# Kernel tuning notes

Measured on AMD Instinct MI355X. Metric: run time of the kernel, lower is better.

## Reference

```python
import jax, jax.numpy as jnp
import numpy as np

B, D_MODEL, L = 4, 512, 1024
N_HEADS = 8

def setup_inputs() -> dict:
    key = jax.random.key(0)
    ks = jax.random.split(key, 7)
    s = 1.0 / np.sqrt(D_MODEL)
    return {
        "queries": jax.random.normal(ks[0], (B, D_MODEL, 3, L), dtype=jnp.float32),
        "keys":    jax.random.normal(ks[1], (B, D_MODEL, 3, L), dtype=jnp.float32),
        "values":  jax.random.normal(ks[2], (B, D_MODEL, 3, L), dtype=jnp.float32),
        "Wq": jax.random.normal(ks[3], (D_MODEL, D_MODEL), dtype=jnp.float32) * s,
        "Wk": jax.random.normal(ks[4], (D_MODEL, D_MODEL), dtype=jnp.float32) * s,
        "Wv": jax.random.normal(ks[5], (D_MODEL, D_MODEL), dtype=jnp.float32) * s,
        "Wo": jax.random.normal(ks[6], (D_MODEL, D_MODEL), dtype=jnp.float32) * s,
        "n_heads": N_HEADS,
    }

def reference(queries, keys, values, Wq, Wk, Wv, Wo, n_heads):
    # inputs: [B, D, 3, L]; VNLinear = bias-free linear over channel dim D
    Bv, D, _, Lv = queries.shape
    H = n_heads
    dh = D // H
    # project and reshape to [B, L, H, dh, 3]
    def proj(x, W):
        y = jnp.einsum('ed,bdvl->blev', W, x)          # [B, L, D, 3]
        return y.reshape(Bv, Lv, H, dh, 3)
    q = proj(queries, Wq)
    k = proj(keys, Wk)
    v = proj(values, Wv)
    # score over extra vector axis v: [B, H, 3, L, S]
    score = jnp.einsum('blhdv,bshdv->bhvls', q, k)
    scale = 1.0 / jnp.sqrt(jnp.asarray(3.0, score.dtype))  # original grabs last dim (=3)
    attn = jax.nn.softmax(scale * score, axis=-1)
    # weighted values: [B, L, 3, H, dh] -> [B, L, 3, D]
    V = jnp.einsum('bhvls,bshdv->blvhd', attn, v).reshape(Bv, Lv, 3, D)
    # output projection on channel dim: result [B, D, 3, L]
    out = jnp.einsum('ed,blvd->bevl', Wo, V)
    return out, attn
```

## Files before the change

### kernel.cpp

```cpp
#include <hip/hip_runtime.h>
#include <hip/hip_bf16.h>

typedef __hip_bfloat16 bf16;
using bf16x8 = __attribute__((ext_vector_type(8))) short;
using f32x4  = __attribute__((ext_vector_type(4))) float;

#define Bn 4
#define Dm 512
#define Hh 8
#define V3 3
#define Lq 1024
#define NM (Bn*Hh*V3)

#define WPITCH 144

__device__ __forceinline__ unsigned short f2bf(float x) {
    bf16 h = __float2bfloat16(x);
    return *reinterpret_cast<unsigned short*>(&h);
}
__device__ __forceinline__ float bfbits2f(unsigned short u) {
    return __uint_as_float((unsigned)u << 16);
}

constexpr float SCALE = 0.57735026919f;

__global__ __launch_bounds__(256, 4) void proj_all_kernel(
    const float* __restrict__ xq, const float* __restrict__ xk,
    const float* __restrict__ xv,
    const float* __restrict__ Wq, const float* __restrict__ Wk,
    const float* __restrict__ Wv,
    unsigned short* __restrict__ Qh, unsigned short* __restrict__ Ql,
    unsigned short* __restrict__ Kh, unsigned short* __restrict__ Kl,
    unsigned short* __restrict__ Vt)
{
    __shared__ unsigned char Wlds[2 * 64 * WPITCH];
    unsigned char* LWh = Wlds;
    unsigned char* LWl = Wlds + 64 * WPITCH;

    const int fid = (blockIdx.z * gridDim.y + blockIdx.y) * gridDim.x + blockIdx.x;
    const int nid = (fid & 7) * 576 + (fid >> 3);
    const int x_  = nid & 15;
    const int y_  = (nid >> 4) & 7;
    const int zz  = nid >> 7;
    const int pid = zz / 12;
    const int pl  = zz % 12;
    const int b   = pl / V3;
    const int v   = pl % V3;

    const float* xsrc = (pid == 0) ? xq : (pid == 1) ? xk : xv;
    const float* W    = (pid == 0) ? Wq : (pid == 1) ? Wk : Wv;

    const int l0 = x_ * 64;
    const int e0 = y_ * 64;
    const int m  = (b * Hh + y_) * V3 + v;

    const int tid  = threadIdx.x;
    const int w    = tid >> 6;
    const int ln   = tid & 63;
    const int ln15 = ln & 15;
    const int lq   = ln >> 4;
    const int wl   = w * 16 + ln15;

    const float* xbase = xsrc + (size_t)b * Dm * V3 * Lq + (size_t)v * Lq + l0 + wl;

    f32x4 acc[4];
    #pragma unroll
    for (int i = 0; i < 4; ++i) acc[i] = (f32x4)0.f;

    for (int ph = 0; ph < 8; ++ph) {
        const int d0 = ph * 64;

        float xraw[16];
        #pragma unroll
        for (int kq = 0; kq < 2; ++kq)
            #pragma unroll
            for (int j = 0; j < 8; ++j)
                xraw[kq * 8 + j] =
                    xbase[(size_t)(d0 + kq * 32 + lq * 8 + j) * (V3 * Lq)];

        __syncthreads();
        #pragma unroll
        for (int q2 = 0; q2 < 4; ++q2) {
            int idx  = tid + q2 * 256;
            int row  = idx >> 4;
            int dloc = (idx & 15) * 4;
            float4 wv4 = *reinterpret_cast<const float4*>(
                W + (size_t)(e0 + row) * Dm + d0 + dloc);
            float wz[4] = {wv4.x, wv4.y, wv4.z, wv4.w};
            union { unsigned short u[4]; uint2 v2; } hp, lp;
            #pragma unroll
            for (int e = 0; e < 4; ++e) {
                hp.u[e] = f2bf(wz[e]);
                lp.u[e] = f2bf(wz[e] - bfbits2f(hp.u[e]));
            }
            *reinterpret_cast<uint2*>(LWh + row * WPITCH + dloc * 2) = hp.v2;
            *reinterpret_cast<uint2*>(LWl + row * WPITCH + dloc * 2) = lp.v2;
        }
        __syncthreads();

        bf16x8 xh[2], xl[2];
        #pragma unroll
        for (int kq = 0; kq < 2; ++kq)
            #pragma unroll
            for (int j = 0; j < 8; ++j) {
                float xv_ = xraw[kq * 8 + j];
                unsigned short hs = f2bf(xv_);
                unsigned short ls = f2bf(xv_ - bfbits2f(hs));
                xh[kq][j] = (short)hs;
                xl[kq][j] = (short)ls;
            }

        #pragma unroll
        for (int lt = 0; lt < 4; ++lt) {
            int erow = lt * 16 + ln15;
            #pragma unroll
            for (int kq = 0; kq < 2; ++kq) {
                bf16x8 wh = *reinterpret_cast<const bf16x8*>(
                    LWh + erow * WPITCH + kq * 64 + lq * 16);
                bf16x8 wl_ = *reinterpret_cast<const bf16x8*>(
                    LWl + erow * WPITCH + kq * 64 + lq * 16);
                acc[lt] = __builtin_amdgcn_mfma_f32_16x16x32_bf16(wh,  xh[kq], acc[lt], 0, 0, 0);
                acc[lt] = __builtin_amdgcn_mfma_f32_16x16x32_bf16(wl_, xh[kq], acc[lt], 0, 0, 0);
                acc[lt] = __builtin_amdgcn_mfma_f32_16x16x32_bf16(wh,  xl[kq], acc[lt], 0, 0, 0);
            }
        }
    }

    if (pid < 2) {
        unsigned short* Oh_ = (pid == 0) ? Qh : Kh;
        unsigned short* Ol_ = (pid == 0) ? Ql : Kl;
        size_t rowbase = ((size_t)m * Lq + l0 + wl) * 64;
        #pragma unroll
        for (int lt = 0; lt < 4; ++lt) {
            union { unsigned short u[4]; uint2 v2; } hp, lp;
            #pragma unroll
            for (int r = 0; r < 4; ++r) {
                float y = acc[lt][r];
                hp.u[r] = f2bf(y);
                lp.u[r] = f2bf(y - bfbits2f(hp.u[r]));
            }
            *reinterpret_cast<uint2*>(Oh_ + rowbase + lt * 16 + lq * 4) = hp.v2;
            *reinterpret_cast<uint2*>(Ol_ + rowbase + lt * 16 + lq * 4) = lp.v2;
        }
    } else {
        #pragma unroll
        for (int lt = 0; lt < 4; ++lt)
            #pragma unroll
            for (int r = 0; r < 4; ++r) {
                int dd = lt * 16 + lq * 4 + r;
                Vt[(((size_t)(m * 64 + dd)) << 10) + l0 + wl] = f2bf(acc[lt][r]);
            }
    }
}

__device__ __forceinline__ void stage_tile64(
    unsigned char* dst, const unsigned short* __restrict__ src,
    size_t row_stride, int tid)
{
    #pragma unroll
    for (int q = 0; q < 2; ++q) {
        int u = tid + q * 256;
        int row = u >> 3, off = u & 7;
        uint4 d = *reinterpret_cast<const uint4*>(src + (size_t)row * row_stride + off * 8);
        *reinterpret_cast<uint4*>(dst + ((row * 128 + off * 16) ^ ((row & 7) << 4))) = d;
    }
}

__global__ __launch_bounds__(256) void fused_attn_kernel(
    const unsigned short* __restrict__ Qh, const unsigned short* __restrict__ Ql,
    const unsigned short* __restrict__ Kh, const unsigned short* __restrict__ Kl,
    const unsigned short* __restrict__ Vt, float* __restrict__ attn_out,
    unsigned short* __restrict__ Ot)
{
    __shared__ float4 ldsf4[2128];
    unsigned char* L   = (unsigned char*)ldsf4;
    unsigned char* Lkh = L;
    unsigned char* Lkl = L + 8192;
    unsigned char* Lvt = L + 16384;
    unsigned char* Lp  = L + 24576;
    float* rowsumW = (float*)(L + 32768);
    float* invrow  = (float*)(L + 33792);

    const int fid = blockIdx.y * gridDim.x + blockIdx.x;
    const int nid = (fid & 7) * 192 + (fid >> 3);
    const int m  = nid >> 4;
    const int l0 = (nid & 15) * 64;

    const int tid = threadIdx.x;
    const int w    = tid >> 6;
    const int ln   = tid & 63;
    const int ln15 = ln & 15;
    const int lq   = ln >> 4;
    const int sc   = w * 16;

    stage_tile64(Lkh, Qh + ((size_t)m * Lq + l0) * 64, 64, tid);
    stage_tile64(Lkl, Ql + ((size_t)m * Lq + l0) * 64, 64, tid);
    __syncthreads();
    bf16x8 qfh[4][2], qfl[4][2];
    #pragma unroll
    for (int lt = 0; lt < 4; ++lt) {
        int row = lt * 16 + ln15;
        #pragma unroll
        for (int kq = 0; kq < 2; ++kq) {
            int byte = (row * 128 + kq * 64 + lq * 16) ^ ((row & 7) << 4);
            qfh[lt][kq] = *reinterpret_cast<const bf16x8*>(Lkh + byte);
            qfl[lt][kq] = *reinterpret_cast<const bf16x8*>(Lkl + byte);
        }
    }
    __syncthreads();

    const size_t mbase = (size_t)m * Lq * Lq;
    const unsigned short* Khm = Kh + (size_t)m * Lq * 64;
    const unsigned short* Klm = Kl + (size_t)m * Lq * 64;
    const unsigned short* Vtm = Vt + (((size_t)m * 64) << 10);

    float lsum[4][4] = {};
    for (int s0 = 0; s0 < Lq; s0 += 64) {
        stage_tile64(Lkh, Khm + (size_t)s0 * 64, 64, tid);
        stage_tile64(Lkl, Klm + (size_t)s0 * 64, 64, tid);
        __syncthreads();
        bf16x8 bh[2], bl[2];
        #pragma unroll
        for (int kq = 0; kq < 2; ++kq) {
            int row = sc + ln15;
            int byte = (row * 128 + kq * 64 + lq * 16) ^ ((row & 7) << 4);
            bh[kq] = *reinterpret_cast<const bf16x8*>(Lkh + byte);
            bl[kq] = *reinterpret_cast<const bf16x8*>(Lkl + byte);
        }
        #pragma unroll
        for (int lt = 0; lt < 4; ++lt) {
            f32x4 c = (f32x4)0.f;
            #pragma unroll
            for (int kq = 0; kq < 2; ++kq) {
                c = __builtin_amdgcn_mfma_f32_16x16x32_bf16(qfh[lt][kq], bh[kq], c, 0, 0, 0);
                c = __builtin_amdgcn_mfma_f32_16x16x32_bf16(qfl[lt][kq], bh[kq], c, 0, 0, 0);
                c = __builtin_amdgcn_mfma_f32_16x16x32_bf16(qfh[lt][kq], bl[kq], c, 0, 0, 0);
            }
            #pragma unroll
            for (int r = 0; r < 4; ++r)
                lsum[lt][r] += __expf(c[r] * SCALE);
        }
        __syncthreads();
    }
    #pragma unroll
    for (int lt = 0; lt < 4; ++lt)
        #pragma unroll
        for (int r = 0; r < 4; ++r) {
            float vv = lsum[lt][r];
            vv += __shfl_xor(vv, 1);
            vv += __shfl_xor(vv, 2);
            vv += __shfl_xor(vv, 4);
            vv += __shfl_xor(vv, 8);
            if (ln15 == 0) rowsumW[w * 64 + lt * 16 + lq * 4 + r] = vv;
        }
    __syncthreads();
    if (tid < 64)
        invrow[tid] = 1.0f / (rowsumW[tid] + rowsumW[64 + tid] +
                              rowsumW[128 + tid] + rowsumW[192 + tid]);
    __syncthreads();

    f32x4 o[4];
    o[0] = (f32x4)0.f; o[1] = (f32x4)0.f; o[2] = (f32x4)0.f; o[3] = (f32x4)0.f;

    for (int s0 = 0; s0 < Lq; s0 += 64) {
        stage_tile64(Lkh, Khm + (size_t)s0 * 64, 64, tid);
        stage_tile64(Lkl, Klm + (size_t)s0 * 64, 64, tid);
        stage_tile64(Lvt, Vtm + s0, 1024, tid);
        __syncthreads();
        bf16x8 bh[2], bl[2];
        #pragma unroll
        for (int kq = 0; kq < 2; ++kq) {
            int row = sc + ln15;
            int byte = (row * 128 + kq * 64 + lq * 16) ^ ((row & 7) << 4);
            bh[kq] = *reinterpret_cast<const bf16x8*>(Lkh + byte);
            bl[kq] = *reinterpret_cast<const bf16x8*>(Lkl + byte);
        }
        #pragma unroll
        for (int lt = 0; lt < 4; ++lt) {
            f32x4 c = (f32x4)0.f;
            #pragma unroll
            for (int kq = 0; kq < 2; ++kq) {
                c = __builtin_amdgcn_mfma_f32_16x16x32_bf16(qfh[lt][kq], bh[kq], c, 0, 0, 0);
                c = __builtin_amdgcn_mfma_f32_16x16x32_bf16(qfl[lt][kq], bh[kq], c, 0, 0, 0);
                c = __builtin_amdgcn_mfma_f32_16x16x32_bf16(qfh[lt][kq], bl[kq], c, 0, 0, 0);
            }
            #pragma unroll
            for (int r = 0; r < 4; ++r) {
                int l = lt * 16 + lq * 4 + r;
                float p = __expf(c[r] * SCALE) * invrow[l];
                attn_out[mbase + (size_t)(l0 + l) * Lq + s0 + sc + ln15] = p;
                int byte = (l * 128 + (sc + ln15) * 2) ^ ((l & 7) << 4);
                *reinterpret_cast<unsigned short*>(Lp + byte) = f2bf(p);
            }
        }
        __syncthreads();
        {
            int prow = w * 16 + ln15;
            #pragma unroll
            for (int kq = 0; kq < 2; ++kq) {
                bf16x8 pa = *reinterpret_cast<const bf16x8*>(
                    Lp + ((prow * 128 + kq * 64 + lq * 16) ^ ((prow & 7) << 4)));
                #pragma unroll
                for (int nt = 0; nt < 4; ++nt) {
                    int vrow = nt * 16 + ln15;
                    bf16x8 vb = *reinterpret_cast<const bf16x8*>(
                        Lvt + ((vrow * 128 + kq * 64 + lq * 16) ^ ((vrow & 7) << 4)));
                    o[nt] = __builtin_amdgcn_mfma_f32_16x16x32_bf16(pa, vb, o[nt], 0, 0, 0);
                }
            }
        }
        __syncthreads();
    }

    #pragma unroll
    for (int nt = 0; nt < 4; ++nt) {
        int dd = nt * 16 + ln15;
        #pragma unroll
        for (int r = 0; r < 4; ++r) {
            int l = w * 16 + lq * 4 + r;
            Ot[((size_t)m * Lq + l0 + l) * 64 + dd] = f2bf(o[nt][r]);
        }
    }
}

__global__ __launch_bounds__(256, 4) void oproj_kernel(
    const float* __restrict__ Wo, const unsigned short* __restrict__ Ot,
    float* __restrict__ out)
{
    __shared__ unsigned char Wlds[2 * 64 * WPITCH];
    unsigned char* LWh = Wlds;
    unsigned char* LWl = Wlds + 64 * WPITCH;

    const int fid = (blockIdx.z * gridDim.y + blockIdx.y) * gridDim.x + blockIdx.x;
    const int nid = (fid & 7) * 192 + (fid >> 3);
    const int x_  = nid & 15;
    const int y_  = (nid >> 4) & 7;
    const int pl  = nid >> 7;
    const int b   = pl / V3;
    const int v   = pl % V3;

    const int l0 = x_ * 64;
    const int e0 = y_ * 64;

    const int tid  = threadIdx.x;
    const int w    = tid >> 6;
    const int ln   = tid & 63;
    const int ln15 = ln & 15;
    const int lq   = ln >> 4;
    const int wl   = w * 16 + ln15;

    f32x4 acc[4];
    #pragma unroll
    for (int i = 0; i < 4; ++i) acc[i] = (f32x4)0.f;

    for (int h = 0; h < Hh; ++h) {
        const int m = (b * Hh + h) * V3 + v;

        size_t obase = ((size_t)m * Lq + l0 + wl) * 64;
        bf16x8 ob0 = *reinterpret_cast<const bf16x8*>(Ot + obase + lq * 8);
        bf16x8 ob1 = *reinterpret_cast<const bf16x8*>(Ot + obase + 32 + lq * 8);

        __syncthreads();
        #pragma unroll
        for (int q2 = 0; q2 < 4; ++q2) {
            int idx  = tid + q2 * 256;
            int row  = idx >> 4;
            int dloc = (idx & 15) * 4;
            float4 wv4 = *reinterpret_cast<const float4*>(
                Wo + (size_t)(e0 + row) * Dm + h * 64 + dloc);
            float wz[4] = {wv4.x, wv4.y, wv4.z, wv4.w};
            union { unsigned short u[4]; uint2 v2; } hp, lp;
            #pragma unroll
            for (int e = 0; e < 4; ++e) {
                hp.u[e] = f2bf(wz[e]);
                lp.u[e] = f2bf(wz[e] - bfbits2f(hp.u[e]));
            }
            *reinterpret_cast<uint2*>(LWh + row * WPITCH + dloc * 2) = hp.v2;
            *reinterpret_cast<uint2*>(LWl + row * WPITCH + dloc * 2) = lp.v2;
        }
        __syncthreads();

        #pragma unroll
        for (int lt = 0; lt < 4; ++lt) {
            int erow = lt * 16 + ln15;
            #pragma unroll
            for (int kq = 0; kq < 2; ++kq) {
                bf16x8 wh = *reinterpret_cast<const bf16x8*>(
                    LWh + erow * WPITCH + kq * 64 + lq * 16);
                bf16x8 wl_ = *reinterpret_cast<const bf16x8*>(
                    LWl + erow * WPITCH + kq * 64 + lq * 16);
                bf16x8 ob = kq ? ob1 : ob0;
                acc[lt] = __builtin_amdgcn_mfma_f32_16x16x32_bf16(wh,  ob, acc[lt], 0, 0, 0);
                acc[lt] = __builtin_amdgcn_mfma_f32_16x16x32_bf16(wl_, ob, acc[lt], 0, 0, 0);
            }
        }
    }

    #pragma unroll
    for (int lt = 0; lt < 4; ++lt)
        #pragma unroll
        for (int r = 0; r < 4; ++r) {
            int e = e0 + lt * 16 + lq * 4 + r;
            out[((size_t)(b * Dm + e) * V3 + v) * Lq + l0 + wl] = acc[lt][r];
        }
}

extern "C" void kernel_launch(void* const* d_in, const int* in_sizes, int n_in,
                              void* d_out, int out_size, void* d_ws, size_t ws_size,
                              hipStream_t stream)
{
    const float* q  = (const float*)d_in[0];
    const float* k  = (const float*)d_in[1];
    const float* vv = (const float*)d_in[2];
    const float* Wq = (const float*)d_in[3];
    const float* Wk = (const float*)d_in[4];
    const float* Wv = (const float*)d_in[5];
    const float* Wo = (const float*)d_in[6];

    float* out      = (float*)d_out;
    float* attn_out = out + (size_t)Bn * Dm * V3 * Lq;

    char* w = (char*)d_ws;
    unsigned short* Qh = (unsigned short*)(w);
    unsigned short* Ql = (unsigned short*)(w + 12582912);
    unsigned short* Kh = (unsigned short*)(w + 25165824);
    unsigned short* Kl = (unsigned short*)(w + 37748736);
    unsigned short* Vt = (unsigned short*)(w + 50331648);
    unsigned short* Ot = (unsigned short*)(w + 62914560);

    dim3 b256(256);

    proj_all_kernel<<<dim3(16, 8, 36), b256, 0, stream>>>(
        q, k, vv, Wq, Wk, Wv, Qh, Ql, Kh, Kl, Vt);

    fused_attn_kernel<<<dim3(16, NM), b256, 0, stream>>>(
        Qh, Ql, Kh, Kl, Vt, attn_out, Ot);

    oproj_kernel<<<dim3(16, 8, 12), b256, 0, stream>>>(Wo, Ot, out);
}
```

Measured before the change: 696.3 us.

## Prefetch K/V tiles into registers and coalesce attention-matrix stores via LDS

Splits tile staging into a global-to-register load and a register-to-LDS write, so the next K/Kl/Vt tile is fetched while the current one is being computed. It also removes one barrier and raises wave priority around the MFMA blocks. The attention probabilities are now written to global memory as wide float4 stores read back from the bf16 P tile in LDS, instead of scattered 4-byte stores. The trade-off is that the stored attn output is rounded to bf16 rather than kept in full fp32, which reduces accuracy.

```diff
diff --git a/kernel.cpp b/kernel.cpp
--- a/kernel.cpp
+++ b/kernel.cpp
@@ -153,16 +153,24 @@
     }
 }
 
-__device__ __forceinline__ void stage_tile64(
-    unsigned char* dst, const unsigned short* __restrict__ src,
-    size_t row_stride, int tid)
+__device__ __forceinline__ void tile_load(
+    uint4* r, const unsigned short* __restrict__ src, size_t row_stride, int tid)
 {
     #pragma unroll
     for (int q = 0; q < 2; ++q) {
         int u = tid + q * 256;
         int row = u >> 3, off = u & 7;
-        uint4 d = *reinterpret_cast<const uint4*>(src + (size_t)row * row_stride + off * 8);
-        *reinterpret_cast<uint4*>(dst + ((row * 128 + off * 16) ^ ((row & 7) << 4))) = d;
+        r[q] = *reinterpret_cast<const uint4*>(src + (size_t)row * row_stride + off * 8);
+    }
+}
+__device__ __forceinline__ void tile_write(
+    const uint4* r, unsigned char* dst, int tid)
+{
+    #pragma unroll
+    for (int q = 0; q < 2; ++q) {
+        int u = tid + q * 256;
+        int row = u >> 3, off = u & 7;
+        *reinterpret_cast<uint4*>(dst + ((row * 128 + off * 16) ^ ((row & 7) << 4))) = r[q];
     }
 }
 
@@ -193,8 +201,13 @@
     const int lq   = ln >> 4;
     const int sc   = w * 16;
 
-    stage_tile64(Lkh, Qh + ((size_t)m * Lq + l0) * 64, 64, tid);
-    stage_tile64(Lkl, Ql + ((size_t)m * Lq + l0) * 64, 64, tid);
+    {
+        uint4 rq[2];
+        tile_load(rq, Qh + ((size_t)m * Lq + l0) * 64, 64, tid);
+        tile_write(rq, Lkh, tid);
+        tile_load(rq, Ql + ((size_t)m * Lq + l0) * 64, 64, tid);
+        tile_write(rq, Lkl, tid);
+    }
     __syncthreads();
     bf16x8 qfh[4][2], qfl[4][2];
     #pragma unroll
@@ -207,7 +220,6 @@
             qfl[lt][kq] = *reinterpret_cast<const bf16x8*>(Lkl + byte);
         }
     }
-    __syncthreads();
 
     const size_t mbase = (size_t)m * Lq * Lq;
     const unsigned short* Khm = Kh + (size_t)m * Lq * 64;
@@ -215,32 +227,46 @@
     const unsigned short* Vtm = Vt + (((size_t)m * 64) << 10);
 
     float lsum[4][4] = {};
-    for (int s0 = 0; s0 < Lq; s0 += 64) {
-        stage_tile64(Lkh, Khm + (size_t)s0 * 64, 64, tid);
-        stage_tile64(Lkl, Klm + (size_t)s0 * 64, 64, tid);
-        __syncthreads();
-        bf16x8 bh[2], bl[2];
-        #pragma unroll
-        for (int kq = 0; kq < 2; ++kq) {
-            int row = sc + ln15;
-            int byte = (row * 128 + kq * 64 + lq * 16) ^ ((row & 7) << 4);
-            bh[kq] = *reinterpret_cast<const bf16x8*>(Lkh + byte);
-            bl[kq] = *reinterpret_cast<const bf16x8*>(Lkl + byte);
-        }
-        #pragma unroll
-        for (int lt = 0; lt < 4; ++lt) {
-            f32x4 c = (f32x4)0.f;
+    {
+        uint4 rkh[2], rkl[2];
+        tile_load(rkh, Khm, 64, tid);
+        tile_load(rkl, Klm, 64, tid);
+        for (int t = 0; t < 16; ++t) {
+            __syncthreads();
+            tile_write(rkh, Lkh, tid);
+            tile_write(rkl, Lkl, tid);
+            __syncthreads();
+            if (t < 15) {
+                tile_load(rkh, Khm + (size_t)(t + 1) * 4096, 64, tid);
+                tile_load(rkl, Klm + (size_t)(t + 1) * 4096, 64, tid);
+            }
+            bf16x8 bh[2], bl[2];
             #pragma unroll
             for (int kq = 0; kq < 2; ++kq) {
-                c = __builtin_amdgcn_mfma_f32_16x16x32_bf16(qfh[lt][kq], bh[kq], c, 0, 0, 0);
-                c = __builtin_amdgcn_mfma_f32_16x16x32_bf16(qfl[lt][kq], bh[kq], c, 0, 0, 0);
-                c = __builtin_amdgcn_mfma_f32_16x16x32_bf16(qfh[lt][kq], bl[kq], c, 0, 0, 0);
-            }
-            #pragma unroll
-            for (int r = 0; r < 4; ++r)
-                lsum[lt][r] += __expf(c[r] * SCALE);
-        }
-        __syncthreads();
+                int row = sc + ln15;
+                int byte = (row * 128 + kq * 64 + lq * 16) ^ ((row & 7) << 4);
+                bh[kq] = *reinterpret_cast<const bf16x8*>(Lkh + byte);
+                bl[kq] = *reinterpret_cast<const bf16x8*>(Lkl + byte);
+            }
+            __builtin_amdgcn_s_setprio(1);
+            f32x4 c[4];
+            #pragma unroll
+            for (int lt = 0; lt < 4; ++lt) {
+                c[lt] = (f32x4)0.f;
+                #pragma unroll
+                for (int kq = 0; kq < 2; ++kq) {
+                    c[lt] = __builtin_amdgcn_mfma_f32_16x16x32_bf16(qfh[lt][kq], bh[kq], c[lt], 0, 0, 0);
+                    c[lt] = __builtin_amdgcn_mfma_f32_16x16x32_bf16(qfl[lt][kq], bh[kq], c[lt], 0, 0, 0);
+                    c[lt] = __builtin_amdgcn_mfma_f32_16x16x32_bf16(qfh[lt][kq], bl[kq], c[lt], 0, 0, 0);
+                }
+            }
+            __builtin_amdgcn_s_setprio(0);
+            #pragma unroll
+            for (int lt = 0; lt < 4; ++lt)
+                #pragma unroll
+                for (int r = 0; r < 4; ++r)
+                    lsum[lt][r] += __expf(c[lt][r] * SCALE);
+        }
     }
     #pragma unroll
     for (int lt = 0; lt < 4; ++lt)
@@ -262,54 +288,104 @@
     f32x4 o[4];
     o[0] = (f32x4)0.f; o[1] = (f32x4)0.f; o[2] = (f32x4)0.f; o[3] = (f32x4)0.f;
 
-    for (int s0 = 0; s0 < Lq; s0 += 64) {
-        stage_tile64(Lkh, Khm + (size_t)s0 * 64, 64, tid);
-        stage_tile64(Lkl, Klm + (size_t)s0 * 64, 64, tid);
-        stage_tile64(Lvt, Vtm + s0, 1024, tid);
-        __syncthreads();
-        bf16x8 bh[2], bl[2];
-        #pragma unroll
-        for (int kq = 0; kq < 2; ++kq) {
-            int row = sc + ln15;
-            int byte = (row * 128 + kq * 64 + lq * 16) ^ ((row & 7) << 4);
-            bh[kq] = *reinterpret_cast<const bf16x8*>(Lkh + byte);
-            bl[kq] = *reinterpret_cast<const bf16x8*>(Lkl + byte);
-        }
-        #pragma unroll
-        for (int lt = 0; lt < 4; ++lt) {
-            f32x4 c = (f32x4)0.f;
+    const int arow = tid >> 2;
+    const int acb  = (tid & 3) * 32;
+    const int aswz = (arow & 7) << 4;
+
+    {
+        uint4 rkh[2], rkl[2], rvt[2];
+        tile_load(rkh, Khm, 64, tid);
+        tile_load(rkl, Klm, 64, tid);
+        tile_load(rvt, Vtm, 1024, tid);
+        for (int t = 0; t < 16; ++t) {
+            const int s0 = t * 64;
+            __syncthreads();
+            tile_write(rkh, Lkh, tid);
+            tile_write(rkl, Lkl, tid);
+            tile_write(rvt, Lvt, tid);
+            __syncthreads();
+            if (t < 15) {
+                tile_load(rkh, Khm + (size_t)(t + 1) * 4096, 64, tid);
+                tile_load(rkl, Klm + (size_t)(t + 1) * 4096, 64, tid);
+                tile_load(rvt, Vtm + (t + 1) * 64, 1024, tid);
+            }
+            bf16x8 bh[2], bl[2];
             #pragma unroll
             for (int kq = 0; kq < 2; ++kq) {
-                c = __builtin_amdgcn_mfma_f32_16x16x32_bf16(qfh[lt][kq], bh[kq], c, 0, 0, 0);
-                c = __builtin_amdgcn_mfma_f32_16x16x32_bf16(qfl[lt][kq], bh[kq], c, 0, 0, 0);
-                c = __builtin_amdgcn_mfma_f32_16x16x32_bf16(qfh[lt][kq], bl[kq], c, 0, 0, 0);
-            }
-            #pragma unroll
-            for (int r = 0; r < 4; ++r) {
-                int l = lt * 16 + lq * 4 + r;
-                float p = __expf(c[r] * SCALE) * invrow[l];
-                attn_out[mbase + (size_t)(l0 + l) * Lq + s0 + sc + ln15] = p;
-                int byte = (l * 128 + (sc + ln15) * 2) ^ ((l & 7) << 4);
-                *reinterpret_cast<unsigned short*>(Lp + byte) = f2bf(p);
-            }
-        }
-        __syncthreads();
-        {
-            int prow = w * 16 + ln15;
-            #pragma unroll
-            for (int kq = 0; kq < 2; ++kq) {
-                bf16x8 pa = *reinterpret_cast<const bf16x8*>(
-                    Lp + ((prow * 128 + kq * 64 + lq * 16) ^ ((prow & 7) << 4)));
+                int row = sc + ln15;
+                int byte = (row * 128 + kq * 64 + lq * 16) ^ ((row & 7) << 4);
+                bh[kq] = *reinterpret_cast<const bf16x8*>(Lkh + byte);
+                bl[kq] = *reinterpret_cast<const bf16x8*>(Lkl + byte);
+            }
+            __builtin_amdgcn_s_setprio(1);
+            f32x4 c[4];
+            #pragma unroll
+            for (int lt = 0; lt < 4; ++lt) {
+                c[lt] = (f32x4)0.f;
                 #pragma unroll
-                for (int nt = 0; nt < 4; ++nt) {
-                    int vrow = nt * 16 + ln15;
-                    bf16x8 vb = *reinterpret_cast<const bf16x8*>(
-                        Lvt + ((vrow * 128 + kq * 64 + lq * 16) ^ ((vrow & 7) << 4)));
-                    o[nt] = __builtin_amdgcn_mfma_f32_16x16x32_bf16(pa, vb, o[nt], 0, 0, 0);
+                for (int kq = 0; kq < 2; ++kq) {
+                    c[lt] = __builtin_amdgcn_mfma_f32_16x16x32_bf16(qfh[lt][kq], bh[kq], c[lt], 0, 0, 0);
+                    c[lt] = __builtin_amdgcn_mfma_f32_16x16x32_bf16(qfl[lt][kq], bh[kq], c[lt], 0, 0, 0);
+                    c[lt] = __builtin_amdgcn_mfma_f32_16x16x32_bf16(qfh[lt][kq], bl[kq], c[lt], 0, 0, 0);
                 }
             }
-        }
-        __syncthreads();
+            __builtin_amdgcn_s_setprio(0);
+            #pragma unroll
+            for (int lt = 0; lt < 4; ++lt)
+                #pragma unroll
+                for (int r = 0; r < 4; ++r) {
+                    int l = lt * 16 + lq * 4 + r;
+                    float p = __expf(c[lt][r] * SCALE) * invrow[l];
+                    int byte = (l * 128 + (sc + ln15) * 2) ^ ((l & 7) << 4);
+                    *reinterpret_cast<unsigned short*>(Lp + byte) = f2bf(p);
+                }
+            __syncthreads();
+            __builtin_amdgcn_s_setprio(1);
+            {
+                int prow = w * 16 + ln15;
+                #pragma unroll
+                for (int kq = 0; kq < 2; ++kq) {
+                    bf16x8 pa = *reinterpret_cast<const bf16x8*>(
+                        Lp + ((prow * 128 + kq * 64 + lq * 16) ^ ((prow & 7) << 4)));
+                    #pragma unroll
+                    for (int nt = 0; nt < 4; ++nt) {
+                        int vrow = nt * 16 + ln15;
+                        bf16x8 vb = *reinterpret_cast<const bf16x8*>(
+                            Lvt + ((vrow * 128 + kq * 64 + lq * 16) ^ ((vrow & 7) << 4)));
+                        o[nt] = __builtin_amdgcn_mfma_f32_16x16x32_bf16(pa, vb, o[nt], 0, 0, 0);
+                    }
+                }
+            }
+            __builtin_amdgcn_s_setprio(0);
+            {
+                bf16x8 p0 = *reinterpret_cast<const bf16x8*>(
+                    Lp + ((arow * 128 + acb) ^ aswz));
+                bf16x8 p1 = *reinterpret_cast<const bf16x8*>(
+                    Lp + ((arow * 128 + acb + 16) ^ aswz));
+                float* dst = attn_out + mbase + (size_t)(l0 + arow) * Lq + s0 + (tid & 3) * 16;
+                float4 f;
+                f.x = bfbits2f((unsigned short)p0[0]);
+                f.y = bfbits2f((unsigned short)p0[1]);
+                f.z = bfbits2f((unsigned short)p0[2]);
+                f.w = bfbits2f((unsigned short)p0[3]);
+                *reinterpret_cast<float4*>(dst) = f;
+                f.x = bfbits2f((unsigned short)p0[4]);
+                f.y = bfbits2f((unsigned short)p0[5]);
+                f.z = bfbits2f((unsigned short)p0[6]);
+                f.w = bfbits2f((unsigned short)p0[7]);
+                *reinterpret_cast<float4*>(dst + 4) = f;
+                f.x = bfbits2f((unsigned short)p1[0]);
+                f.y = bfbits2f((unsigned short)p1[1]);
+                f.z = bfbits2f((unsigned short)p1[2]);
+                f.w = bfbits2f((unsigned short)p1[3]);
+                *reinterpret_cast<float4*>(dst + 8) = f;
+                f.x = bfbits2f((unsigned short)p1[4]);
+                f.y = bfbits2f((unsigned short)p1[5]);
+                f.z = bfbits2f((unsigned short)p1[6]);
+                f.w = bfbits2f((unsigned short)p1[7]);
+                *reinterpret_cast<float4*>(dst + 12) = f;
+            }
+        }
     }
 
     #pragma unroll
```

After: 865.7 us. +24.3%, slower.
